# Kernel tuning notes

Measured on AMD Instinct MI355X. Metric: run time of the kernel, lower is better.

## Reference

```python
import jax, jax.numpy as jnp
import numpy as np

N = 50000
D = 128
E = 600000
R = 8


def setup_inputs() -> dict:
    key = jax.random.key(0)
    ks = jax.random.split(key, 8)
    x = jax.random.normal(ks[0], (N, D), dtype=jnp.float32)
    edge_index = jax.random.randint(ks[1], (2, E), 0, N, dtype=jnp.int64)
    edge_type = jax.random.randint(ks[2], (E,), 0, R, dtype=jnp.int64)
    scale = 1.0 / np.sqrt(D)
    w1 = jax.random.normal(ks[3], (R, D, D), dtype=jnp.float32) * scale
    root1 = jax.random.normal(ks[4], (D, D), dtype=jnp.float32) * scale
    b1 = jnp.zeros((D,), dtype=jnp.float32)
    w2 = jax.random.normal(ks[5], (R, D, D), dtype=jnp.float32) * scale
    root2 = jax.random.normal(ks[6], (D, D), dtype=jnp.float32) * scale
    b2 = jnp.zeros((D,), dtype=jnp.float32)
    return {"x": x, "edge_index": edge_index, "edge_type": edge_type,
            "w1": w1, "root1": root1, "b1": b1,
            "w2": w2, "root2": root2, "b2": b2}


def _rgcn_conv(x, edge_index, edge_type, w, root, b):
    # PyG RGCNConv: per-relation MEAN aggregation of source features over
    # incoming edges, then relation-specific linear, summed over relations,
    # plus root transform and bias.
    src, dst = edge_index[0], edge_index[1]
    # combined segment id: (dst_node, relation) -> one segment_sum pass
    seg = dst * R + edge_type  # [E]
    msgs = x[src]              # [E, D] gather
    sums = jax.ops.segment_sum(msgs, seg, num_segments=N * R).reshape(N, R, D)
    cnts = jax.ops.segment_sum(jnp.ones((msgs.shape[0],), dtype=x.dtype), seg,
                               num_segments=N * R).reshape(N, R, 1)
    mean = sums / jnp.maximum(cnts, 1.0)  # [N, R, D]; empty -> 0
    out = jnp.einsum('nrd,rde->ne', mean, w) + x @ root + b
    return out


def reference(x, edge_index, edge_type, w1, root1, b1, w2, root2, b2):
    # dropout is identity in eval mode
    h = jax.nn.relu(_rgcn_conv(x, edge_index, edge_type, w1, root1, b1))
    out = jax.nn.relu(_rgcn_conv(h, edge_index, edge_type, w2, root2, b2))
    return out
```

## Files before the change

kernel.cpp:

```cpp
#include <hip/hip_runtime.h>

#define NN 50000
#define D 128
#define EE 600000
#define R 8
#define NR (NN * R)
#define SCAN_CHUNK 1024
#define NSB ((NR + SCAN_CHUNK - 1) / SCAN_CHUNK)
#define KT 36

typedef unsigned short u16;
typedef unsigned int u32;
typedef __attribute__((ext_vector_type(8))) short bf16x8;
typedef __attribute__((ext_vector_type(4))) float f32x4;

#define RDL(v_, i_) __builtin_amdgcn_readlane((int)(v_), (i_))

__device__ inline u16 f2bf(float f) {
    union { float f; u32 u; } v; v.f = f;
    return (u16)((v.u + 0x7FFFu + ((v.u >> 16) & 1u)) >> 16);
}
__device__ inline float bf2f(u16 h) {
    union { u32 u; float f; } v; v.u = ((u32)h) << 16;
    return v.f;
}

__global__ __launch_bounds__(256) void histrank_kernel(const int* __restrict__ dst,
                                                       const int* __restrict__ et,
                                                       int* __restrict__ cnt,
                                                       int* __restrict__ rk, int E) {
    int e = blockIdx.x * 256 + threadIdx.x;
    if (e < E) rk[e] = atomicAdd(&cnt[dst[e] * R + et[e]], 1);
}

__global__ __launch_bounds__(256) void scanA(const int* __restrict__ cnt,
                                             int* __restrict__ off,
                                             int* __restrict__ bsum) {
    __shared__ int ts[256];
    const int b = blockIdx.x, t = threadIdx.x;
    const int base = b * SCAN_CHUNK + t * 4;
    int v0 = 0, v1 = 0, v2 = 0, v3 = 0;
    if (base + 3 < NR) {
        int4 q = *(const int4*)(cnt + base);
        v0 = q.x; v1 = q.y; v2 = q.z; v3 = q.w;
    } else {
        if (base < NR) v0 = cnt[base];
        if (base + 1 < NR) v1 = cnt[base + 1];
        if (base + 2 < NR) v2 = cnt[base + 2];
    }
    const int s = v0 + v1 + v2 + v3;
    ts[t] = s;
    __syncthreads();
    for (int d = 1; d < 256; d <<= 1) {
        int x = (t >= d) ? ts[t - d] : 0;
        __syncthreads();
        ts[t] += x;
        __syncthreads();
    }
    const int excl = ts[t] - s;
    if (base < NR) off[base] = excl;
    if (base + 1 < NR) off[base + 1] = excl + v0;
    if (base + 2 < NR) off[base + 2] = excl + v0 + v1;
    if (base + 3 < NR) off[base + 3] = excl + v0 + v1 + v2;
    if (t == 255) bsum[b] = ts[255];
}

__global__ __launch_bounds__(256) void scanBC(int* __restrict__ off,
                                              const int* __restrict__ bsum) {
    __shared__ int red[256];
    const int b = blockIdx.x, t = threadIdx.x;
    int p = 0;
    for (int i = t; i < b; i += 256) p += bsum[i];
    red[t] = p;
    __syncthreads();
    for (int d = 128; d > 0; d >>= 1) {
        if (t < d) red[t] += red[t + d];
        __syncthreads();
    }
    const int add = red[0];
    const int base = b * SCAN_CHUNK + t * 4;
#pragma unroll
    for (int j = 0; j < 4; ++j)
        if (base + j < NR) off[base + j] += add;
    if (b == 0 && t == 0) off[NR] = EE;
}

__global__ __launch_bounds__(256) void place2_kernel(const int* __restrict__ src,
                                                     const int* __restrict__ dst,
                                                     const int* __restrict__ et,
                                                     const int* __restrict__ off,
                                                     const int* __restrict__ rk,
                                                     u32* __restrict__ epk, int E) {
    int e = blockIdx.x * 256 + threadIdx.x;
    if (e < E) {
        const int r = et[e];
        const int p = off[dst[e] * R + r] + rk[e];
        epk[p] = ((u32)src[e] << 3) | (u32)r;
    }
}

__global__ __launch_bounds__(256) void bprep2_kernel(const float* __restrict__ w1,
                                                     const float* __restrict__ root1,
                                                     u16* __restrict__ Bf1,
                                                     const float* __restrict__ w2,
                                                     const float* __restrict__ root2,
                                                     u16* __restrict__ Bf2,
                                                     int4* __restrict__ cntz) {
    int gidx = blockIdx.x * 256 + threadIdx.x;
    for (int i = gidx; i < NR / 4; i += 36864)
        cntz[i] = make_int4(0, 0, 0, 0);
    if (gidx >= 2 * KT * 8 * 64) return;
    const int layer = gidx / (KT * 8 * 64);
    const int idx = gidx - layer * (KT * 8 * 64);
    const float* w = layer ? w2 : w1;
    const float* root = layer ? root2 : root1;
    u16* Bfrag = layer ? Bf2 : Bf1;
    const int lane = idx & 63;
    const int g = (idx >> 6) & 7;
    const int kt = idx >> 9;
    const int col = g * 16 + (lane & 15);
    const int kbase = kt * 32 + (lane >> 4) * 8;
    u16* o = Bfrag + (size_t)idx * 8;
#pragma unroll
    for (int j = 0; j < 8; ++j) {
        const int k = kbase + j;
        float v = (k < R * D) ? w[(size_t)(k >> 7) * (D * D) + (size_t)(k & 127) * D + col]
                              : root[(size_t)(k - R * D) * D + col];
        o[j] = f2bf(v);
    }
}

__global__ __launch_bounds__(256) void xcast_kernel(const float4* __restrict__ x,
                                                    u32* __restrict__ xb) {
    int i = blockIdx.x * 256 + threadIdx.x;
    if (i < NN * 32) {
        float4 v = x[i];
        xb[i * 2] = (u32)f2bf(v.x) | ((u32)f2bf(v.y) << 16);
        xb[i * 2 + 1] = (u32)f2bf(v.z) | ((u32)f2bf(v.w) << 16);
    }
}

template <bool OUTBF>
__global__ __launch_bounds__(512, 4) void rgcn_fused(const u32* __restrict__ xb,
                                                     const u16* __restrict__ Bf,
                                                     const int* __restrict__ off,
                                                     const u32* __restrict__ epk,
                                                     const float* __restrict__ bias,
                                                     void* __restrict__ outp) {
    __shared__ u32 A32[KT * 2 * 256];

    const int t = threadIdx.x;
    const int wid = t >> 6;
    const int lane = t & 63;
    const int n0 = blockIdx.x * 32;

    const int q2 = (lane & 15) >> 2;
    const int ktl = lane >> 4;
    const int xv = q2 | ((ktl & 1) << 2);

    {
        uint4* Az = (uint4*)A32;
        for (int i = t; i < (KT * 2 * 256) / 4; i += 512)
            Az[i] = make_uint4(0, 0, 0, 0);
    }
    __syncthreads();

    const int i0 = wid * 4;
    const int nb = n0 + i0;

    int offv;
    {
        int oi = nb * 8 + lane;
        if (oi > NR) oi = NR;
        offv = off[oi];
    }
    const int e0 = RDL(offv, 0);
    const int e1 = RDL(offv, 32);

    u32 rv0, rv1, rv2, rv3;
    {
        int c0 = (nb < NN) ? nb : (NN - 1);
        int c1 = (nb + 1 < NN) ? nb + 1 : (NN - 1);
        int c2 = (nb + 2 < NN) ? nb + 2 : (NN - 1);
        int c3 = (nb + 3 < NN) ? nb + 3 : (NN - 1);
        rv0 = xb[(size_t)c0 * 64 + lane];
        rv1 = xb[(size_t)c1 * 64 + lane];
        rv2 = xb[(size_t)c2 * 64 + lane];
        rv3 = xb[(size_t)c3 * 64 + lane];
    }

    int wb = e0;
    u32 w0, w1;
    {
        int ia = e0 + lane; if (ia >= EE) ia = EE - 1;
        int ib = e0 + 64 + lane; if (ib >= EE) ib = EE - 1;
        w0 = epk[ia];
        w1 = epk[ib];
    }

    int seg = 0;
    while (seg < 32 && RDL(offv, seg + 1) <= e0) ++seg;
    int segEnd = (seg < 32) ? RDL(offv, seg + 1) : 0x7FFFFFFF;
    int segStart = e0;
    float sx = 0.f, sy = 0.f;

#define FLUSH(pp)                                                              \
    do {                                                                       \
        const float inv_ = 1.f / (float)((pp) - segStart);                     \
        const int i_ = i0 + (seg >> 3);                                        \
        const int mt_ = i_ >> 4;                                               \
        const int wb_ = ((((i_ & 15) ^ xv) + 16 * q2) << 2) + (lane & 3);      \
        A32[(((seg & 7) * 4 + ktl) * 2 + mt_) * 256 + wb_] =                   \
            (u32)f2bf(sx * inv_) | ((u32)f2bf(sy * inv_) << 16);               \
        sx = 0.f; sy = 0.f; segStart = (pp);                                   \
        ++seg;                                                                 \
        while (seg < 32 && RDL(offv, seg + 1) <= (pp)) ++seg;                  \
        segEnd = (seg < 32) ? RDL(offv, seg + 1) : 0x7FFFFFFF;                 \
    } while (0)

#define PREF1(d_, pp)                                                          \
    do {                                                                       \
        const int j_ = (pp) - wb;                                              \
        const u32 pk_ = (u32)((j_ < 64) ? RDL(w0, j_) : RDL(w1, j_ - 64));     \
        d_ = xb[(size_t)(pk_ >> 3) * 64 + lane];                               \
    } while (0)

#define PROC1(v_, pp)                                                          \
    do {                                                                       \
        if ((pp) == segEnd) FLUSH(pp);                                         \
        if ((pp) < e1) {                                                       \
            sx += bf2f((u16)((v_) & 0xFFFFu));                                 \
            sy += bf2f((u16)((v_) >> 16));                                     \
        }                                                                      \
    } while (0)

    int p = e0;
    u32 a0, a1, a2, a3, b0, b1, b2, b3, c0, c1, c2, c3;
    PREF1(a0, p);     PREF1(a1, p + 1); PREF1(a2, p + 2); PREF1(a3, p + 3);
    PREF1(b0, p + 4); PREF1(b1, p + 5); PREF1(b2, p + 6); PREF1(b3, p + 7);
    const int nbt = (e1 - e0 + 3) >> 2;
#pragma unroll 1
    for (int bt = 0; bt < nbt; ++bt) {
        if (p + 8 - wb >= 64) {
            wb += 64; w0 = w1;
            int ia = wb + 64 + lane; if (ia >= EE) ia = EE - 1;
            w1 = epk[ia];
        }
        PREF1(c0, p + 8); PREF1(c1, p + 9); PREF1(c2, p + 10); PREF1(c3, p + 11);
        PROC1(a0, p); PROC1(a1, p + 1); PROC1(a2, p + 2); PROC1(a3, p + 3);
        p += 4;
        a0 = b0; a1 = b1; a2 = b2; a3 = b3;
        b0 = c0; b1 = c1; b2 = c2; b3 = c3;
    }
    if (seg < 32 && segStart < e1) FLUSH(e1);

#undef FLUSH
#undef PREF1
#undef PROC1

    {
#pragma unroll
        for (int k = 0; k < 4; ++k) {
            const int ii = i0 + k;
            const int mt_ = ii >> 4;
            const int wb_ = ((((ii & 15) ^ xv) + 16 * q2) << 2) + (lane & 3);
            const u32 rv = (k == 0) ? rv0 : (k == 1) ? rv1 : (k == 2) ? rv2 : rv3;
            A32[((32 + ktl) * 2 + mt_) * 256 + wb_] = rv;
        }
    }
    __syncthreads();

    const int g = wid;
    f32x4 accL = {0.f, 0.f, 0.f, 0.f}, accH = {0.f, 0.f, 0.f, 0.f};
    const u16* bp = Bf + ((size_t)g * 64 + lane) * 8;
    const u16* A16 = (const u16*)A32;
#pragma unroll 4
    for (int kt = 0; kt < KT; ++kt) {
        const bf16x8 b = *(const bf16x8*)(bp + (size_t)kt * 4096);
        const int xvr = (lane >> 4) | ((kt & 1) << 2);
        const int lp = (lane ^ xvr) * 8;
        const bf16x8 fa0 = *(const bf16x8*)(A16 + (kt * 2 + 0) * 512 + lp);
        const bf16x8 fa1 = *(const bf16x8*)(A16 + (kt * 2 + 1) * 512 + lp);
        accL = __builtin_amdgcn_mfma_f32_16x16x32_bf16(fa0, b, accL, 0, 0, 0);
        accH = __builtin_amdgcn_mfma_f32_16x16x32_bf16(fa1, b, accH, 0, 0, 0);
    }

    const int quad = lane >> 4;
    const int l15 = lane & 15;
    const int col = g * 16 + l15;
    const float bb = bias[col];
#pragma unroll
    for (int q = 0; q < 4; ++q) {
        const int rL = n0 + quad * 4 + q;
        const int rH = rL + 16;
        const float vL = fmaxf(accL[q] + bb, 0.f);
        const float vH = fmaxf(accH[q] + bb, 0.f);
        if (OUTBF) {
            u16* hp = (u16*)outp;
            if (rL < NN) hp[(size_t)rL * D + col] = f2bf(vL);
            if (rH < NN) hp[(size_t)rH * D + col] = f2bf(vH);
        } else {
            float* op = (float*)outp;
            if (rL < NN) op[(size_t)rL * D + col] = vL;
            if (rH < NN) op[(size_t)rH * D + col] = vH;
        }
    }
}

extern "C" void kernel_launch(void* const* d_in, const int* in_sizes, int n_in,
                              void* d_out, int out_size, void* d_ws, size_t ws_size,
                              hipStream_t stream) {
    const float* x = (const float*)d_in[0];
    const int* ei = (const int*)d_in[1];
    const int* et = (const int*)d_in[2];
    const float* w1 = (const float*)d_in[3];
    const float* root1 = (const float*)d_in[4];
    const float* b1 = (const float*)d_in[5];
    const float* w2 = (const float*)d_in[6];
    const float* root2 = (const float*)d_in[7];
    const float* b2 = (const float*)d_in[8];
    float* out = (float*)d_out;

    char* ws = (char*)d_ws;
    int* off    = (int*)(ws + 0);
    int* cnt_i  = (int*)(ws + 1600512);
    int* rk     = (int*)(ws + 3200512);
    int* bsum   = (int*)(ws + 5600512);
    u32* epk    = (u32*)(ws + 5604096);
    u32* xb     = (u32*)(ws + 8004096);
    u32* h      = (u32*)(ws + 20804096);
    u16* Bf1    = (u16*)(ws + 33604096);
    u16* Bf2    = (u16*)(ws + 33899008);

    const int* srcp = ei;
    const int* dstp = ei + EE;

    bprep2_kernel<<<144, 256, 0, stream>>>(w1, root1, Bf1, w2, root2, Bf2,
                                           (int4*)cnt_i);
    xcast_kernel<<<(NN * 32 + 255) / 256, 256, 0, stream>>>((const float4*)x, xb);
    histrank_kernel<<<(EE + 255) / 256, 256, 0, stream>>>(dstp, et, cnt_i, rk, EE);
    scanA<<<NSB, 256, 0, stream>>>(cnt_i, off, bsum);
    scanBC<<<NSB, 256, 0, stream>>>(off, bsum);
    place2_kernel<<<(EE + 255) / 256, 256, 0, stream>>>(srcp, dstp, et, off, rk,
                                                        epk, EE);

    const int fused_blocks = (NN + 31) / 32;

    rgcn_fused<true><<<fused_blocks, 512, 0, stream>>>(xb, Bf1, off, epk, b1,
                                                       (void*)h);
    rgcn_fused<false><<<fused_blocks, 512, 0, stream>>>(h, Bf2, off, epk, b2,
                                                        (void*)out);
}
```

Before: 285.3 us.

## Halve node tile per block, merge xcast and histogram kernels, simplify bf16 unpack

```diff
diff --git a/kernel.cpp b/kernel.cpp
--- a/kernel.cpp
+++ b/kernel.cpp
@@ -25,12 +25,17 @@
     return v.f;
 }
 
-__global__ __launch_bounds__(256) void histrank_kernel(const int* __restrict__ dst,
-                                                       const int* __restrict__ et,
-                                                       int* __restrict__ cnt,
-                                                       int* __restrict__ rk, int E) {
-    int e = blockIdx.x * 256 + threadIdx.x;
-    if (e < E) rk[e] = atomicAdd(&cnt[dst[e] * R + et[e]], 1);
+__global__ __launch_bounds__(256) void prep2_kernel(const float4* __restrict__ x,
+                                                    u32* __restrict__ xb,
+                                                    const int* __restrict__ dst,
+                                                    const int* __restrict__ et,
+                                                    int* __restrict__ cnt,
+                                                    int* __restrict__ rk) {
+    const int i = blockIdx.x * 256 + threadIdx.x;
+    const float4 v = x[i];
+    if (i < EE) rk[i] = atomicAdd(&cnt[dst[i] * R + et[i]], 1);
+    xb[i * 2] = (u32)f2bf(v.x) | ((u32)f2bf(v.y) << 16);
+    xb[i * 2 + 1] = (u32)f2bf(v.z) | ((u32)f2bf(v.w) << 16);
 }
 
 __global__ __launch_bounds__(256) void scanA(const int* __restrict__ cnt,
@@ -130,29 +135,19 @@
     }
 }
 
-__global__ __launch_bounds__(256) void xcast_kernel(const float4* __restrict__ x,
-                                                    u32* __restrict__ xb) {
-    int i = blockIdx.x * 256 + threadIdx.x;
-    if (i < NN * 32) {
-        float4 v = x[i];
-        xb[i * 2] = (u32)f2bf(v.x) | ((u32)f2bf(v.y) << 16);
-        xb[i * 2 + 1] = (u32)f2bf(v.z) | ((u32)f2bf(v.w) << 16);
-    }
-}
-
 template <bool OUTBF>
-__global__ __launch_bounds__(512, 4) void rgcn_fused(const u32* __restrict__ xb,
+__global__ __launch_bounds__(512, 8) void rgcn_fused(const u32* __restrict__ xb,
                                                      const u16* __restrict__ Bf,
                                                      const int* __restrict__ off,
                                                      const u32* __restrict__ epk,
                                                      const float* __restrict__ bias,
                                                      void* __restrict__ outp) {
-    __shared__ u32 A32[KT * 2 * 256];
+    __shared__ u32 A32[KT * 256];
 
     const int t = threadIdx.x;
     const int wid = t >> 6;
     const int lane = t & 63;
-    const int n0 = blockIdx.x * 32;
+    const int n0 = blockIdx.x * 16;
 
     const int q2 = (lane & 15) >> 2;
     const int ktl = lane >> 4;
@@ -160,12 +155,12 @@
 
     {
         uint4* Az = (uint4*)A32;
-        for (int i = t; i < (KT * 2 * 256) / 4; i += 512)
+        for (int i = t; i < (KT * 256) / 4; i += 512)
             Az[i] = make_uint4(0, 0, 0, 0);
     }
     __syncthreads();
 
-    const int i0 = wid * 4;
+    const int i0 = wid * 2;
     const int nb = n0 + i0;
 
     int offv;
@@ -175,19 +170,10 @@
         offv = off[oi];
     }
     const int e0 = RDL(offv, 0);
-    const int e1 = RDL(offv, 32);
-
-    u32 rv0, rv1, rv2, rv3;
-    {
-        int c0 = (nb < NN) ? nb : (NN - 1);
-        int c1 = (nb + 1 < NN) ? nb + 1 : (NN - 1);
-        int c2 = (nb + 2 < NN) ? nb + 2 : (NN - 1);
-        int c3 = (nb + 3 < NN) ? nb + 3 : (NN - 1);
-        rv0 = xb[(size_t)c0 * 64 + lane];
-        rv1 = xb[(size_t)c1 * 64 + lane];
-        rv2 = xb[(size_t)c2 * 64 + lane];
-        rv3 = xb[(size_t)c3 * 64 + lane];
-    }
+    const int e1 = RDL(offv, 16);
+
+    const u32 rv0 = xb[(size_t)nb * 64 + lane];
+    const u32 rv1 = xb[(size_t)(nb + 1) * 64 + lane];
 
     int wb = e0;
     u32 w0, w1;
@@ -199,8 +185,8 @@
     }
 
     int seg = 0;
-    while (seg < 32 && RDL(offv, seg + 1) <= e0) ++seg;
-    int segEnd = (seg < 32) ? RDL(offv, seg + 1) : 0x7FFFFFFF;
+    while (seg < 16 && RDL(offv, seg + 1) <= e0) ++seg;
+    int segEnd = (seg < 16) ? RDL(offv, seg + 1) : 0x7FFFFFFF;
     int segStart = e0;
     float sx = 0.f, sy = 0.f;
 
@@ -208,14 +194,13 @@
     do {                                                                       \
         const float inv_ = 1.f / (float)((pp) - segStart);                     \
         const int i_ = i0 + (seg >> 3);                                        \
-        const int mt_ = i_ >> 4;                                               \
-        const int wb_ = ((((i_ & 15) ^ xv) + 16 * q2) << 2) + (lane & 3);      \
-        A32[(((seg & 7) * 4 + ktl) * 2 + mt_) * 256 + wb_] =                   \
+        const int wb_ = (((i_ ^ xv) + 16 * q2) << 2) + (lane & 3);             \
+        A32[((seg & 7) * 4 + ktl) * 256 + wb_] =                               \
             (u32)f2bf(sx * inv_) | ((u32)f2bf(sy * inv_) << 16);               \
         sx = 0.f; sy = 0.f; segStart = (pp);                                   \
         ++seg;                                                                 \
-        while (seg < 32 && RDL(offv, seg + 1) <= (pp)) ++seg;                  \
-        segEnd = (seg < 32) ? RDL(offv, seg + 1) : 0x7FFFFFFF;                 \
+        while (seg < 16 && RDL(offv, seg + 1) <= (pp)) ++seg;                  \
+        segEnd = (seg < 16) ? RDL(offv, seg + 1) : 0x7FFFFFFF;                 \
     } while (0)
 
 #define PREF1(d_, pp)                                                          \
@@ -229,8 +214,11 @@
     do {                                                                       \
         if ((pp) == segEnd) FLUSH(pp);                                         \
         if ((pp) < e1) {                                                       \
-            sx += bf2f((u16)((v_) & 0xFFFFu));                                 \
-            sy += bf2f((u16)((v_) >> 16));                                     \
+            union { u32 u; float f; } lo_, hi_;                                \
+            lo_.u = (v_) << 16;                                                \
+            hi_.u = (v_) & 0xFFFF0000u;                                        \
+            sx += lo_.f;                                                       \
+            sy += hi_.f;                                                       \
         }                                                                      \
     } while (0)
 
@@ -252,26 +240,22 @@
         a0 = b0; a1 = b1; a2 = b2; a3 = b3;
         b0 = c0; b1 = c1; b2 = c2; b3 = c3;
     }
-    if (seg < 32 && segStart < e1) FLUSH(e1);
+    if (seg < 16 && segStart < e1) FLUSH(e1);
 
 #undef FLUSH
 #undef PREF1
 #undef PROC1
 
     {
-#pragma unroll
-        for (int k = 0; k < 4; ++k) {
-            const int ii = i0 + k;
-            const int mt_ = ii >> 4;
-            const int wb_ = ((((ii & 15) ^ xv) + 16 * q2) << 2) + (lane & 3);
-            const u32 rv = (k == 0) ? rv0 : (k == 1) ? rv1 : (k == 2) ? rv2 : rv3;
-            A32[((32 + ktl) * 2 + mt_) * 256 + wb_] = rv;
-        }
+        const int wb0 = (((i0 ^ xv) + 16 * q2) << 2) + (lane & 3);
+        const int wb1 = ((((i0 + 1) ^ xv) + 16 * q2) << 2) + (lane & 3);
+        A32[(32 + ktl) * 256 + wb0] = rv0;
+        A32[(32 + ktl) * 256 + wb1] = rv1;
     }
     __syncthreads();
 
     const int g = wid;
-    f32x4 accL = {0.f, 0.f, 0.f, 0.f}, accH = {0.f, 0.f, 0.f, 0.f};
+    f32x4 acc = {0.f, 0.f, 0.f, 0.f};
     const u16* bp = Bf + ((size_t)g * 64 + lane) * 8;
     const u16* A16 = (const u16*)A32;
 #pragma unroll 4
@@ -279,10 +263,8 @@
         const bf16x8 b = *(const bf16x8*)(bp + (size_t)kt * 4096);
         const int xvr = (lane >> 4) | ((kt & 1) << 2);
         const int lp = (lane ^ xvr) * 8;
-        const bf16x8 fa0 = *(const bf16x8*)(A16 + (kt * 2 + 0) * 512 + lp);
-        const bf16x8 fa1 = *(const bf16x8*)(A16 + (kt * 2 + 1) * 512 + lp);
-        accL = __builtin_amdgcn_mfma_f32_16x16x32_bf16(fa0, b, accL, 0, 0, 0);
-        accH = __builtin_amdgcn_mfma_f32_16x16x32_bf16(fa1, b, accH, 0, 0, 0);
+        const bf16x8 fa = *(const bf16x8*)(A16 + kt * 512 + lp);
+        acc = __builtin_amdgcn_mfma_f32_16x16x32_bf16(fa, b, acc, 0, 0, 0);
     }
 
     const int quad = lane >> 4;
@@ -291,19 +273,12 @@
     const float bb = bias[col];
 #pragma unroll
     for (int q = 0; q < 4; ++q) {
-        const int rL = n0 + quad * 4 + q;
-        const int rH = rL + 16;
-        const float vL = fmaxf(accL[q] + bb, 0.f);
-        const float vH = fmaxf(accH[q] + bb, 0.f);
-        if (OUTBF) {
-            u16* hp = (u16*)outp;
-            if (rL < NN) hp[(size_t)rL * D + col] = f2bf(vL);
-            if (rH < NN) hp[(size_t)rH * D + col] = f2bf(vH);
-        } else {
-            float* op = (float*)outp;
-            if (rL < NN) op[(size_t)rL * D + col] = vL;
-            if (rH < NN) op[(size_t)rH * D + col] = vH;
-        }
+        const int row = n0 + quad * 4 + q;
+        const float v = fmaxf(acc[q] + bb, 0.f);
+        if (OUTBF)
+            ((u16*)outp)[(size_t)row * D + col] = f2bf(v);
+        else
+            ((float*)outp)[(size_t)row * D + col] = v;
     }
 }
 
@@ -337,14 +312,14 @@
 
     bprep2_kernel<<<144, 256, 0, stream>>>(w1, root1, Bf1, w2, root2, Bf2,
                                            (int4*)cnt_i);
-    xcast_kernel<<<(NN * 32 + 255) / 256, 256, 0, stream>>>((const float4*)x, xb);
-    histrank_kernel<<<(EE + 255) / 256, 256, 0, stream>>>(dstp, et, cnt_i, rk, EE);
+    prep2_kernel<<<NN * 32 / 256, 256, 0, stream>>>((const float4*)x, xb,
+                                                    dstp, et, cnt_i, rk);
     scanA<<<NSB, 256, 0, stream>>>(cnt_i, off, bsum);
     scanBC<<<NSB, 256, 0, stream>>>(off, bsum);
     place2_kernel<<<(EE + 255) / 256, 256, 0, stream>>>(srcp, dstp, et, off, rk,
                                                         epk, EE);
 
-    const int fused_blocks = (NN + 31) / 32;
+    const int fused_blocks = NN / 16;
 
     rgcn_fused<true><<<fused_blocks, 512, 0, stream>>>(xb, Bf1, off, epk, b1,
                                                        (void*)h);
```

Result: faster. 252.4 us (-11.5%).
